# Kernel optimization log

Measured on AMD Instinct MI355X. Metric: run time of the kernel, lower is better.

## Reference

```python
import jax, jax.numpy as jnp
import numpy as np


def setup_inputs() -> dict:
    key = jax.random.key(0)
    ks = jax.random.split(key, 7)
    N, T, E = 4, 2048, 1024
    s = 1.0 / np.sqrt(E)
    return {
        "X": jax.random.normal(ks[0], (N, T, E), dtype=jnp.float32),
        "Wq": jax.random.normal(ks[1], (E, E), dtype=jnp.float32) * s,
        "bq": jax.random.normal(ks[2], (E,), dtype=jnp.float32) * 0.01,
        "Wk": jax.random.normal(ks[3], (E, E), dtype=jnp.float32) * s,
        "bk": jax.random.normal(ks[4], (E,), dtype=jnp.float32) * 0.01,
        "Wv": jax.random.normal(ks[5], (E, E), dtype=jnp.float32) * s,
        "bv": jax.random.normal(ks[6], (E,), dtype=jnp.float32) * 0.01,
    }


def reference(X, Wq, bq, Wk, bk, Wv, bv):
    # QKV projections: [N,T,E] @ [E,E] + [E]
    q = jnp.einsum("nte,ef->ntf", X, Wq) + bq
    k = jnp.einsum("nte,ef->ntf", X, Wk) + bk
    v = jnp.einsum("nte,ef->ntf", X, Wv) + bv
    # Unscaled full attention (module does NOT divide by sqrt(E))
    sim = jnp.einsum("nqe,nke->nqk", q, k)         # [N,T,T]
    weight = jax.nn.softmax(sim, axis=2)
    return jnp.einsum("nqk,nke->nqe", weight, v)    # [N,T,E]
```

## Files before the change

kernel.cpp:

```cpp
#include <hip/hip_runtime.h>

typedef unsigned short u16;
typedef unsigned int u32;
typedef float floatx4 __attribute__((ext_vector_type(4)));
typedef __bf16 bf16x8 __attribute__((ext_vector_type(8)));

__device__ __forceinline__ u16 bf16_rne(float x) {
  u32 u = __builtin_bit_cast(u32, x);
  return (u16)((u + 0x7FFFu + ((u >> 16) & 1u)) >> 16);
}
__device__ __forceinline__ float bf16f(u16 h) {
  u32 u = ((u32)h) << 16;
  return __builtin_bit_cast(float, u);
}
__device__ __forceinline__ void g2l16(const u16* g, u16* l) {
  __builtin_amdgcn_global_load_lds((const __attribute__((address_space(1))) u32*)g,
                                   (__attribute__((address_space(3))) u32*)l, 16, 0, 0);
}
__device__ __forceinline__ floatx4 mfma16(bf16x8 a, bf16x8 b, floatx4 c) {
  return __builtin_amdgcn_mfma_f32_16x16x32_bf16(a, b, c, 0, 0, 0);
}
#define SB() __builtin_amdgcn_sched_barrier(0)

__global__ void split_x_kernel(const float* __restrict__ X, u16* __restrict__ Xh,
                               u16* __restrict__ Xl, int n4) {
  int i = blockIdx.x * blockDim.x + threadIdx.x;
  int stride = gridDim.x * blockDim.x;
  for (; i < n4; i += stride) {
    float4 x = reinterpret_cast<const float4*>(X)[i];
    float v[4] = {x.x, x.y, x.z, x.w};
    u16 hh[4], ll[4];
#pragma unroll
    for (int j = 0; j < 4; ++j) {
      hh[j] = bf16_rne(v[j]);
      ll[j] = bf16_rne(v[j] - bf16f(hh[j]));
    }
    reinterpret_cast<ushort4*>(Xh)[i] = make_ushort4(hh[0], hh[1], hh[2], hh[3]);
    reinterpret_cast<ushort4*>(Xl)[i] = make_ushort4(ll[0], ll[1], ll[2], ll[3]);
  }
}

__global__ void wsplit_t_kernel(const float* __restrict__ W, u16* __restrict__ Th,
                                u16* __restrict__ Tl) {
  __shared__ float tile[32][33];
  int tx = threadIdx.x, ty = threadIdx.y;
  int f0 = blockIdx.x * 32, e0 = blockIdx.y * 32;
  tile[ty][tx] = W[(e0 + ty) * 1024 + f0 + tx];
  __syncthreads();
  float v = tile[tx][ty];
  u16 h = bf16_rne(v);
  Th[(f0 + ty) * 1024 + e0 + tx] = h;
  Tl[(f0 + ty) * 1024 + e0 + tx] = bf16_rne(v - bf16f(h));
}

template <int EPI>
__global__ __launch_bounds__(512, 2) void gemm8_split(
    const u16* __restrict__ Ah, const u16* __restrict__ Al,
    const u16* __restrict__ Bh, const u16* __restrict__ Bl,
    float* __restrict__ C, u16* __restrict__ Oh, u16* __restrict__ Ol,
    const float* __restrict__ b1, const float* __restrict__ b2, int NH,
    int N, int K, int lda, int ldb, long sA, long sB, long sC) {
  __shared__ u16 lds[2][4][256 * 32];
  const int tid = threadIdx.x;
  const int z = blockIdx.z;
  const int brow = blockIdx.y * 256;
  const int bcol = blockIdx.x * 256;
  const int w = tid >> 6, l = tid & 63;
  const int wm = w >> 2, wn = w & 3;
  const int fr = l & 15, kq = l >> 4;

  const u16* gA0 = Ah + (long)z * sA + (long)brow * lda;
  const u16* gA1 = Al + (long)z * sA + (long)brow * lda;
  const u16* gB0 = Bh + (long)z * sB + (long)bcol * ldb;
  const u16* gB1 = Bl + (long)z * sB + (long)bcol * ldb;

  const int r0 = tid >> 2, s0 = tid & 3;
  const int r1 = (tid + 512) >> 2, s1 = (tid + 512) & 3;
  const long aOff0 = (long)r0 * lda + ((s0 ^ ((r0 >> 1) & 3)) << 3);
  const long aOff1 = (long)r1 * lda + ((s1 ^ ((r1 >> 1) & 3)) << 3);
  const long bOff0 = (long)r0 * ldb + ((s0 ^ ((r0 >> 1) & 3)) << 3);
  const long bOff1 = (long)r1 * ldb + ((s1 ^ ((r1 >> 1) & 3)) << 3);
  const int d0 = tid * 8, d1 = (tid + 512) * 8;

  auto STAGE = [&](int b, int k0) {
    g2l16(gA0 + aOff0 + k0, &lds[b][0][d0]);
    g2l16(gA0 + aOff1 + k0, &lds[b][0][d1]);
    g2l16(gA1 + aOff0 + k0, &lds[b][1][d0]);
    g2l16(gA1 + aOff1 + k0, &lds[b][1][d1]);
    g2l16(gB0 + bOff0 + k0, &lds[b][2][d0]);
    g2l16(gB0 + bOff1 + k0, &lds[b][2][d1]);
    g2l16(gB1 + bOff0 + k0, &lds[b][3][d0]);
    g2l16(gB1 + bOff1 + k0, &lds[b][3][d1]);
  };

  int aoffs[8], boffs[4];
#pragma unroll
  for (int m = 0; m < 8; ++m) {
    int r = wm * 128 + m * 16 + fr;
    aoffs[m] = r * 32 + (((kq ^ (r >> 1)) & 3) << 3);
  }
#pragma unroll
  for (int n = 0; n < 4; ++n) {
    int r = wn * 64 + n * 16 + fr;
    boffs[n] = r * 32 + (((kq ^ (r >> 1)) & 3) << 3);
  }

  floatx4 acc[8][4];
#pragma unroll
  for (int m = 0; m < 8; ++m)
#pragma unroll
    for (int n = 0; n < 4; ++n)
#pragma unroll
      for (int j = 0; j < 4; ++j) acc[m][n][j] = 0.f;

  const int NT = K >> 5;
  STAGE(0, 0);
  STAGE(1, 32);
  SB();
  asm volatile("s_waitcnt vmcnt(8)" ::: "memory");
  SB(); __builtin_amdgcn_s_barrier(); SB();

  bf16x8 fa_h[4], fa_l[4], fb_h[4], fb_l[4];

  for (int t = 0; t < NT; ++t) {
    const int p = t & 1;
    const u16* LAh = &lds[p][0][0];
    const u16* LAl = &lds[p][1][0];
    const u16* LBh = &lds[p][2][0];
    const u16* LBl = &lds[p][3][0];

#pragma unroll
    for (int m = 0; m < 4; ++m) {
      fa_h[m] = *(const bf16x8*)(LAh + aoffs[m]);
      fa_l[m] = *(const bf16x8*)(LAl + aoffs[m]);
    }
#pragma unroll
    for (int n = 0; n < 2; ++n) {
      fb_h[n] = *(const bf16x8*)(LBh + boffs[n]);
      fb_l[n] = *(const bf16x8*)(LBl + boffs[n]);
    }
    SB(); __builtin_amdgcn_s_barrier();
    asm volatile("s_waitcnt lgkmcnt(0)" ::: "memory");
    SB();
    __builtin_amdgcn_s_setprio(1);
#pragma unroll
    for (int m = 0; m < 4; ++m)
#pragma unroll
      for (int n = 0; n < 2; ++n) {
        acc[m][n] = mfma16(fa_h[m], fb_h[n], acc[m][n]);
        acc[m][n] = mfma16(fa_h[m], fb_l[n], acc[m][n]);
        acc[m][n] = mfma16(fa_l[m], fb_h[n], acc[m][n]);
      }
    __builtin_amdgcn_s_setprio(0);
    SB(); __builtin_amdgcn_s_barrier(); SB();

#pragma unroll
    for (int n = 2; n < 4; ++n) {
      fb_h[n] = *(const bf16x8*)(LBh + boffs[n]);
      fb_l[n] = *(const bf16x8*)(LBl + boffs[n]);
    }
    SB(); __builtin_amdgcn_s_barrier();
    asm volatile("s_waitcnt lgkmcnt(0)" ::: "memory");
    SB();
    __builtin_amdgcn_s_setprio(1);
#pragma unroll
    for (int m = 0; m < 4; ++m)
#pragma unroll
      for (int n = 2; n < 4; ++n) {
        acc[m][n] = mfma16(fa_h[m], fb_h[n], acc[m][n]);
        acc[m][n] = mfma16(fa_h[m], fb_l[n], acc[m][n]);
        acc[m][n] = mfma16(fa_l[m], fb_h[n], acc[m][n]);
      }
    __builtin_amdgcn_s_setprio(0);
    SB(); __builtin_amdgcn_s_barrier(); SB();

#pragma unroll
    for (int m = 0; m < 4; ++m) {
      fa_h[m] = *(const bf16x8*)(LAh + aoffs[m + 4]);
      fa_l[m] = *(const bf16x8*)(LAl + aoffs[m + 4]);
    }
    SB(); __builtin_amdgcn_s_barrier();
    asm volatile("s_waitcnt lgkmcnt(0)" ::: "memory");
    SB();
    __builtin_amdgcn_s_setprio(1);
#pragma unroll
    for (int m = 0; m < 4; ++m)
#pragma unroll
      for (int n = 0; n < 2; ++n) {
        acc[m + 4][n] = mfma16(fa_h[m], fb_h[n], acc[m + 4][n]);
        acc[m + 4][n] = mfma16(fa_h[m], fb_l[n], acc[m + 4][n]);
        acc[m + 4][n] = mfma16(fa_l[m], fb_h[n], acc[m + 4][n]);
      }
    __builtin_amdgcn_s_setprio(0);
    SB(); __builtin_amdgcn_s_barrier(); SB();

    if (t + 2 < NT) STAGE(p, (t + 2) << 5);
    SB();
    __builtin_amdgcn_s_setprio(1);
#pragma unroll
    for (int m = 0; m < 4; ++m)
#pragma unroll
      for (int n = 2; n < 4; ++n) {
        acc[m + 4][n] = mfma16(fa_h[m], fb_h[n], acc[m + 4][n]);
        acc[m + 4][n] = mfma16(fa_h[m], fb_l[n], acc[m + 4][n]);
        acc[m + 4][n] = mfma16(fa_l[m], fb_h[n], acc[m + 4][n]);
      }
    __builtin_amdgcn_s_setprio(0);
    SB();
    if (t + 2 < NT) {
      asm volatile("s_waitcnt vmcnt(8)" ::: "memory");
    } else {
      asm volatile("s_waitcnt vmcnt(0)" ::: "memory");
    }
    SB(); __builtin_amdgcn_s_barrier(); SB();
  }

#pragma unroll
  for (int m = 0; m < 8; ++m)
#pragma unroll
    for (int n = 0; n < 4; ++n)
#pragma unroll
      for (int j = 0; j < 4; ++j) {
        int gr = brow + wm * 128 + m * 16 + kq * 4 + j;
        int gc = bcol + wn * 64 + n * 16 + fr;
        float v = acc[m][n][j];
        if (EPI == 0) {
          C[(long)z * sC + (long)gr * N + gc] = v;
        } else {
          v += (gc < NH) ? b1[gc] : b2[gc - NH];
          u16 h = bf16_rne(v);
          long idx = (long)gr * N + gc;
          Oh[idx] = h;
          Ol[idx] = bf16_rne(v - bf16f(h));
        }
      }
}

template <int EPI>
__global__ __launch_bounds__(512, 2) void gemm8_plain(
    const u16* __restrict__ A, const u16* __restrict__ B,
    float* __restrict__ C, u16* __restrict__ Oh, const float* __restrict__ bias,
    int N, int K, int lda, int ldb, long sA, long sB, long sC) {
  __shared__ u16 lds[2][24576];
  const int BOFF = 16384;
  const int tid = threadIdx.x;
  const int z = blockIdx.z;
  const int brow = blockIdx.y * 256;
  const int bcol = blockIdx.x * 128;
  const int w = tid >> 6, l = tid & 63;
  const int wm = w >> 2, wn = w & 3;
  const int fr = l & 15, kq = l >> 4;

  const u16* gA = A + (long)z * sA + (long)brow * lda;
  const u16* gB = B + (long)z * sB + (long)bcol * ldb;

  long aO[4], bO[2];
  int aD[4], bD[2];
#pragma unroll
  for (int i = 0; i < 4; ++i) {
    int c = tid + i * 512, r = c >> 3, s = c & 7;
    aO[i] = (long)r * lda + ((s ^ (r & 7)) << 3);
    aD[i] = c * 8;
  }
#pragma unroll
  for (int i = 0; i < 2; ++i) {
    int c = tid + i * 512, r = c >> 3, s = c & 7;
    bO[i] = (long)r * ldb + ((s ^ (r & 7)) << 3);
    bD[i] = BOFF + c * 8;
  }

  auto STAGE = [&](int b, int k0) {
#pragma unroll
    for (int i = 0; i < 4; ++i) g2l16(gA + aO[i] + k0, &lds[b][aD[i]]);
#pragma unroll
    for (int i = 0; i < 2; ++i) g2l16(gB + bO[i] + k0, &lds[b][bD[i]]);
  };

  int aoffs[8][2], boffs[2][2];
#pragma unroll
  for (int m = 0; m < 8; ++m) {
    int r = wm * 128 + m * 16 + fr;
#pragma unroll
    for (int k = 0; k < 2; ++k) aoffs[m][k] = r * 64 + ((((k * 4 + kq) ^ r) & 7) << 3);
  }
#pragma unroll
  for (int n = 0; n < 2; ++n) {
    int r = wn * 32 + n * 16 + fr;
#pragma unroll
    for (int k = 0; k < 2; ++k) boffs[n][k] = BOFF + r * 64 + ((((k * 4 + kq) ^ r) & 7) << 3);
  }

  floatx4 acc[8][2];
#pragma unroll
  for (int m = 0; m < 8; ++m)
#pragma unroll
    for (int n = 0; n < 2; ++n)
#pragma unroll
      for (int j = 0; j < 4; ++j) acc[m][n][j] = 0.f;

  const int NT = K >> 6;
  STAGE(0, 0);
  STAGE(1, 64);
  SB();
  asm volatile("s_waitcnt vmcnt(6)" ::: "memory");
  SB(); __builtin_amdgcn_s_barrier(); SB();

  bf16x8 fak[4][2], fb[2][2];

  for (int t = 0; t < NT; ++t) {
    const int p = t & 1;
    const u16* L = &lds[p][0];

#pragma unroll
    for (int m = 0; m < 4; ++m)
#pragma unroll
      for (int k = 0; k < 2; ++k) fak[m][k] = *(const bf16x8*)(L + aoffs[m][k]);
#pragma unroll
    for (int n = 0; n < 2; ++n)
#pragma unroll
      for (int k = 0; k < 2; ++k) fb[n][k] = *(const bf16x8*)(L + boffs[n][k]);
    SB(); __builtin_amdgcn_s_barrier();
    asm volatile("s_waitcnt lgkmcnt(0)" ::: "memory");
    SB();
    __builtin_amdgcn_s_setprio(1);
#pragma unroll
    for (int m = 0; m < 4; ++m)
#pragma unroll
      for (int n = 0; n < 2; ++n) {
        acc[m][n] = mfma16(fak[m][0], fb[n][0], acc[m][n]);
        acc[m][n] = mfma16(fak[m][1], fb[n][1], acc[m][n]);
      }
    __builtin_amdgcn_s_setprio(0);
    SB(); __builtin_amdgcn_s_barrier(); SB();

#pragma unroll
    for (int m = 0; m < 4; ++m)
#pragma unroll
      for (int k = 0; k < 2; ++k) fak[m][k] = *(const bf16x8*)(L + aoffs[m + 4][k]);
    SB(); __builtin_amdgcn_s_barrier();
    asm volatile("s_waitcnt lgkmcnt(0)" ::: "memory");
    SB();
    __builtin_amdgcn_s_setprio(1);
#pragma unroll
    for (int m = 0; m < 4; ++m)
#pragma unroll
      for (int n = 0; n < 2; ++n)
        acc[m + 4][n] = mfma16(fak[m][0], fb[n][0], acc[m + 4][n]);
    __builtin_amdgcn_s_setprio(0);
    SB(); __builtin_amdgcn_s_barrier(); SB();

    if (t + 2 < NT) STAGE(p, (t + 2) << 6);
    SB();
    __builtin_amdgcn_s_setprio(1);
#pragma unroll
    for (int m = 0; m < 4; ++m)
#pragma unroll
      for (int n = 0; n < 2; ++n)
        acc[m + 4][n] = mfma16(fak[m][1], fb[n][1], acc[m + 4][n]);
    __builtin_amdgcn_s_setprio(0);
    SB();
    if (t + 2 < NT) {
      asm volatile("s_waitcnt vmcnt(6)" ::: "memory");
    } else {
      asm volatile("s_waitcnt vmcnt(0)" ::: "memory");
    }
    SB(); __builtin_amdgcn_s_barrier(); SB();
  }

#pragma unroll
  for (int m = 0; m < 8; ++m)
#pragma unroll
    for (int n = 0; n < 2; ++n)
#pragma unroll
      for (int j = 0; j < 4; ++j) {
        int gr = brow + wm * 128 + m * 16 + kq * 4 + j;
        int gc = bcol + wn * 32 + n * 16 + fr;
        float v = acc[m][n][j];
        if (EPI == 0) {
          C[(long)z * sC + (long)gr * N + gc] = v;
        } else {
          v += bias[gc];
          long oi = ((long)((gr >> 11) * 1024 + gc)) * 2048 + (gr & 2047);
          Oh[oi] = bf16_rne(v);
        }
      }
}

__global__ __launch_bounds__(256) void softmax_kernel(const float* __restrict__ S,
                                                      u16* __restrict__ Wgt) {
  const long row = blockIdx.x;
  const float4* src = reinterpret_cast<const float4*>(S + row * 2048);
  const int t = threadIdx.x;
  float4 x0 = src[t];
  float4 x1 = src[t + 256];
  float m = fmaxf(fmaxf(fmaxf(x0.x, x0.y), fmaxf(x0.z, x0.w)),
                  fmaxf(fmaxf(x1.x, x1.y), fmaxf(x1.z, x1.w)));
#pragma unroll
  for (int s = 32; s > 0; s >>= 1) m = fmaxf(m, __shfl_xor(m, s));
  __shared__ float redm[4];
  __shared__ float reds[4];
  if ((t & 63) == 0) redm[t >> 6] = m;
  __syncthreads();
  m = fmaxf(fmaxf(redm[0], redm[1]), fmaxf(redm[2], redm[3]));
  float e[8];
  e[0] = __expf(x0.x - m); e[1] = __expf(x0.y - m);
  e[2] = __expf(x0.z - m); e[3] = __expf(x0.w - m);
  e[4] = __expf(x1.x - m); e[5] = __expf(x1.y - m);
  e[6] = __expf(x1.z - m); e[7] = __expf(x1.w - m);
  float s = ((e[0] + e[1]) + (e[2] + e[3])) + ((e[4] + e[5]) + (e[6] + e[7]));
#pragma unroll
  for (int k = 32; k > 0; k >>= 1) s += __shfl_xor(s, k);
  if ((t & 63) == 0) reds[t >> 6] = s;
  __syncthreads();
  s = (reds[0] + reds[1]) + (reds[2] + reds[3]);
  float inv = 1.f / s;
  u32* dst = reinterpret_cast<u32*>(Wgt + row * 2048);
  dst[2 * t] = (u32)bf16_rne(e[0] * inv) | ((u32)bf16_rne(e[1] * inv) << 16);
  dst[2 * t + 1] = (u32)bf16_rne(e[2] * inv) | ((u32)bf16_rne(e[3] * inv) << 16);
  dst[2 * (t + 256)] = (u32)bf16_rne(e[4] * inv) | ((u32)bf16_rne(e[5] * inv) << 16);
  dst[2 * (t + 256) + 1] = (u32)bf16_rne(e[6] * inv) | ((u32)bf16_rne(e[7] * inv) << 16);
}

extern "C" void kernel_launch(void* const* d_in, const int* in_sizes, int n_in,
                              void* d_out, int out_size, void* d_ws, size_t ws_size,
                              hipStream_t stream) {
  const float* X = (const float*)d_in[0];
  const float* Wq = (const float*)d_in[1];
  const float* bq = (const float*)d_in[2];
  const float* Wk = (const float*)d_in[3];
  const float* bk = (const float*)d_in[4];
  const float* Wv = (const float*)d_in[5];
  const float* bv = (const float*)d_in[6];
  float* out = (float*)d_out;

  char* ws = (char*)d_ws;
  const size_t MB = 1ull << 20;
  u16* Xh = (u16*)(ws + 0 * MB);
  u16* Xl = (u16*)(ws + 16 * MB);
  u16* Wqkh = (u16*)(ws + 32 * MB);
  u16* Wqkl = (u16*)(ws + 36 * MB);
  u16* Wvh = (u16*)(ws + 40 * MB);
  u16* Wvl = (u16*)(ws + 42 * MB);
  float* sim = (float*)(ws);
  u16* qkh = (u16*)(ws + 64 * MB);
  u16* qkl = (u16*)(ws + 96 * MB);
  u16* vt = (u16*)(ws + 128 * MB);
  u16* wb = (u16*)(ws + 64 * MB);

  split_x_kernel<<<4096, 256, 0, stream>>>(X, Xh, Xl, (8192 * 1024) / 4);
  wsplit_t_kernel<<<dim3(32, 32), dim3(32, 32), 0, stream>>>(Wq, Wqkh, Wqkl);
  wsplit_t_kernel<<<dim3(32, 32), dim3(32, 32), 0, stream>>>(Wk, Wqkh + 1024 * 1024,
                                                             Wqkl + 1024 * 1024);
  wsplit_t_kernel<<<dim3(32, 32), dim3(32, 32), 0, stream>>>(Wv, Wvh, Wvl);
  gemm8_split<1><<<dim3(8, 32, 1), 512, 0, stream>>>(
      Xh, Xl, Wqkh, Wqkl, nullptr, qkh, qkl, bq, bk, 1024,
      2048, 1024, 1024, 1024, 0, 0, 0);
  gemm8_plain<2><<<dim3(8, 32, 1), 512, 0, stream>>>(
      Xh, Wvh, nullptr, vt, bv, 1024, 1024, 1024, 1024, 0, 0, 0);
  gemm8_split<0><<<dim3(8, 8, 4), 512, 0, stream>>>(
      qkh, qkl, qkh + 1024, qkl + 1024, sim, nullptr, nullptr, nullptr, nullptr, 0,
      2048, 1024, 2048, 2048, 2048L * 2048, 2048L * 2048, 2048L * 2048);
  softmax_kernel<<<8192, 256, 0, stream>>>(sim, wb);
  gemm8_plain<0><<<dim3(8, 8, 4), 512, 0, stream>>>(
      wb, vt, out, nullptr, nullptr, 1024, 2048, 2048, 2048,
      2048L * 2048, 1024L * 2048, 2048L * 1024);
}
```

Before: 378.2 us.

## Reshape plain GEMM tiles to 128x256, add XCD block swizzle, reorder MFMAs

```diff
diff --git a/kernel.cpp b/kernel.cpp
--- a/kernel.cpp
+++ b/kernel.cpp
@@ -21,6 +21,21 @@
   return __builtin_amdgcn_mfma_f32_16x16x32_bf16(a, b, c, 0, 0, 0);
 }
 #define SB() __builtin_amdgcn_sched_barrier(0)
+
+__device__ __forceinline__ void xcd_swizzle(int& bx, int& by, int& bz) {
+  const int gx = gridDim.x, gy = gridDim.y;
+  int nb = gx * gy * gridDim.z;
+  int flat = blockIdx.x + gx * (blockIdx.y + gy * blockIdx.z);
+  int swz = flat;
+  if ((nb & 7) == 0) {
+    int cpx = nb >> 3;
+    swz = (flat & 7) * cpx + (flat >> 3);
+  }
+  bz = swz / (gx * gy);
+  int rem = swz - bz * gx * gy;
+  by = rem / gx;
+  bx = rem - by * gx;
+}
 
 __global__ void split_x_kernel(const float* __restrict__ X, u16* __restrict__ Xh,
                                u16* __restrict__ Xl, int n4) {
@@ -62,9 +77,11 @@
     int N, int K, int lda, int ldb, long sA, long sB, long sC) {
   __shared__ u16 lds[2][4][256 * 32];
   const int tid = threadIdx.x;
-  const int z = blockIdx.z;
-  const int brow = blockIdx.y * 256;
-  const int bcol = blockIdx.x * 256;
+  int bx, by, bz;
+  xcd_swizzle(bx, by, bz);
+  const int z = bz;
+  const int brow = by * 256;
+  const int bcol = bx * 256;
   const int w = tid >> 6, l = tid & 63;
   const int wm = w >> 2, wn = w & 3;
   const int fr = l & 15, kq = l >> 4;
@@ -146,11 +163,15 @@
 #pragma unroll
     for (int m = 0; m < 4; ++m)
 #pragma unroll
-      for (int n = 0; n < 2; ++n) {
-        acc[m][n] = mfma16(fa_h[m], fb_h[n], acc[m][n]);
-        acc[m][n] = mfma16(fa_h[m], fb_l[n], acc[m][n]);
-        acc[m][n] = mfma16(fa_l[m], fb_h[n], acc[m][n]);
-      }
+      for (int n = 0; n < 2; ++n) acc[m][n] = mfma16(fa_h[m], fb_h[n], acc[m][n]);
+#pragma unroll
+    for (int m = 0; m < 4; ++m)
+#pragma unroll
+      for (int n = 0; n < 2; ++n) acc[m][n] = mfma16(fa_h[m], fb_l[n], acc[m][n]);
+#pragma unroll
+    for (int m = 0; m < 4; ++m)
+#pragma unroll
+      for (int n = 0; n < 2; ++n) acc[m][n] = mfma16(fa_l[m], fb_h[n], acc[m][n]);
     __builtin_amdgcn_s_setprio(0);
     SB(); __builtin_amdgcn_s_barrier(); SB();
 
@@ -166,11 +187,15 @@
 #pragma unroll
     for (int m = 0; m < 4; ++m)
 #pragma unroll
-      for (int n = 2; n < 4; ++n) {
-        acc[m][n] = mfma16(fa_h[m], fb_h[n], acc[m][n]);
-        acc[m][n] = mfma16(fa_h[m], fb_l[n], acc[m][n]);
-        acc[m][n] = mfma16(fa_l[m], fb_h[n], acc[m][n]);
-      }
+      for (int n = 2; n < 4; ++n) acc[m][n] = mfma16(fa_h[m], fb_h[n], acc[m][n]);
+#pragma unroll
+    for (int m = 0; m < 4; ++m)
+#pragma unroll
+      for (int n = 2; n < 4; ++n) acc[m][n] = mfma16(fa_h[m], fb_l[n], acc[m][n]);
+#pragma unroll
+    for (int m = 0; m < 4; ++m)
+#pragma unroll
+      for (int n = 2; n < 4; ++n) acc[m][n] = mfma16(fa_l[m], fb_h[n], acc[m][n]);
     __builtin_amdgcn_s_setprio(0);
     SB(); __builtin_amdgcn_s_barrier(); SB();
 
@@ -186,11 +211,15 @@
 #pragma unroll
     for (int m = 0; m < 4; ++m)
 #pragma unroll
-      for (int n = 0; n < 2; ++n) {
-        acc[m + 4][n] = mfma16(fa_h[m], fb_h[n], acc[m + 4][n]);
-        acc[m + 4][n] = mfma16(fa_h[m], fb_l[n], acc[m + 4][n]);
-        acc[m + 4][n] = mfma16(fa_l[m], fb_h[n], acc[m + 4][n]);
-      }
+      for (int n = 0; n < 2; ++n) acc[m + 4][n] = mfma16(fa_h[m], fb_h[n], acc[m + 4][n]);
+#pragma unroll
+    for (int m = 0; m < 4; ++m)
+#pragma unroll
+      for (int n = 0; n < 2; ++n) acc[m + 4][n] = mfma16(fa_h[m], fb_l[n], acc[m + 4][n]);
+#pragma unroll
+    for (int m = 0; m < 4; ++m)
+#pragma unroll
+      for (int n = 0; n < 2; ++n) acc[m + 4][n] = mfma16(fa_l[m], fb_h[n], acc[m + 4][n]);
     __builtin_amdgcn_s_setprio(0);
     SB(); __builtin_amdgcn_s_barrier(); SB();
 
@@ -200,11 +229,15 @@
 #pragma unroll
     for (int m = 0; m < 4; ++m)
 #pragma unroll
-      for (int n = 2; n < 4; ++n) {
-        acc[m + 4][n] = mfma16(fa_h[m], fb_h[n], acc[m + 4][n]);
-        acc[m + 4][n] = mfma16(fa_h[m], fb_l[n], acc[m + 4][n]);
-        acc[m + 4][n] = mfma16(fa_l[m], fb_h[n], acc[m + 4][n]);
-      }
+      for (int n = 2; n < 4; ++n) acc[m + 4][n] = mfma16(fa_h[m], fb_h[n], acc[m + 4][n]);
+#pragma unroll
+    for (int m = 0; m < 4; ++m)
+#pragma unroll
+      for (int n = 2; n < 4; ++n) acc[m + 4][n] = mfma16(fa_h[m], fb_l[n], acc[m + 4][n]);
+#pragma unroll
+    for (int m = 0; m < 4; ++m)
+#pragma unroll
+      for (int n = 2; n < 4; ++n) acc[m + 4][n] = mfma16(fa_l[m], fb_h[n], acc[m + 4][n]);
     __builtin_amdgcn_s_setprio(0);
     SB();
     if (t + 2 < NT) {
@@ -242,28 +275,30 @@
     float* __restrict__ C, u16* __restrict__ Oh, const float* __restrict__ bias,
     int N, int K, int lda, int ldb, long sA, long sB, long sC) {
   __shared__ u16 lds[2][24576];
-  const int BOFF = 16384;
+  const int BOFF = 8192;
   const int tid = threadIdx.x;
-  const int z = blockIdx.z;
-  const int brow = blockIdx.y * 256;
-  const int bcol = blockIdx.x * 128;
+  int bx, by, bz;
+  xcd_swizzle(bx, by, bz);
+  const int z = bz;
+  const int brow = by * 128;
+  const int bcol = bx * 256;
   const int w = tid >> 6, l = tid & 63;
-  const int wm = w >> 2, wn = w & 3;
+  const int wm = (w >> 2) * 64, wn = (w & 3) * 64;
   const int fr = l & 15, kq = l >> 4;
 
   const u16* gA = A + (long)z * sA + (long)brow * lda;
   const u16* gB = B + (long)z * sB + (long)bcol * ldb;
 
-  long aO[4], bO[2];
-  int aD[4], bD[2];
-#pragma unroll
-  for (int i = 0; i < 4; ++i) {
+  long aO[2], bO[4];
+  int aD[2], bD[4];
+#pragma unroll
+  for (int i = 0; i < 2; ++i) {
     int c = tid + i * 512, r = c >> 3, s = c & 7;
     aO[i] = (long)r * lda + ((s ^ (r & 7)) << 3);
     aD[i] = c * 8;
   }
 #pragma unroll
-  for (int i = 0; i < 2; ++i) {
+  for (int i = 0; i < 4; ++i) {
     int c = tid + i * 512, r = c >> 3, s = c & 7;
     bO[i] = (long)r * ldb + ((s ^ (r & 7)) << 3);
     bD[i] = BOFF + c * 8;
@@ -271,30 +306,30 @@
 
   auto STAGE = [&](int b, int k0) {
 #pragma unroll
-    for (int i = 0; i < 4; ++i) g2l16(gA + aO[i] + k0, &lds[b][aD[i]]);
-#pragma unroll
-    for (int i = 0; i < 2; ++i) g2l16(gB + bO[i] + k0, &lds[b][bD[i]]);
+    for (int i = 0; i < 2; ++i) g2l16(gA + aO[i] + k0, &lds[b][aD[i]]);
+#pragma unroll
+    for (int i = 0; i < 4; ++i) g2l16(gB + bO[i] + k0, &lds[b][bD[i]]);
   };
 
-  int aoffs[8][2], boffs[2][2];
-#pragma unroll
-  for (int m = 0; m < 8; ++m) {
-    int r = wm * 128 + m * 16 + fr;
+  int aoffs[4][2], boffs[4][2];
+#pragma unroll
+  for (int m = 0; m < 4; ++m) {
+    int r = wm + m * 16 + fr;
 #pragma unroll
     for (int k = 0; k < 2; ++k) aoffs[m][k] = r * 64 + ((((k * 4 + kq) ^ r) & 7) << 3);
   }
 #pragma unroll
-  for (int n = 0; n < 2; ++n) {
-    int r = wn * 32 + n * 16 + fr;
+  for (int n = 0; n < 4; ++n) {
+    int r = wn + n * 16 + fr;
 #pragma unroll
     for (int k = 0; k < 2; ++k) boffs[n][k] = BOFF + r * 64 + ((((k * 4 + kq) ^ r) & 7) << 3);
   }
 
-  floatx4 acc[8][2];
-#pragma unroll
-  for (int m = 0; m < 8; ++m)
-#pragma unroll
-    for (int n = 0; n < 2; ++n)
+  floatx4 acc[4][4];
+#pragma unroll
+  for (int m = 0; m < 4; ++m)
+#pragma unroll
+    for (int n = 0; n < 4; ++n)
 #pragma unroll
       for (int j = 0; j < 4; ++j) acc[m][n][j] = 0.f;
 
@@ -305,16 +340,16 @@
   asm volatile("s_waitcnt vmcnt(6)" ::: "memory");
   SB(); __builtin_amdgcn_s_barrier(); SB();
 
-  bf16x8 fak[4][2], fb[2][2];
+  bf16x8 fa[2][2], fb[4][2];
 
   for (int t = 0; t < NT; ++t) {
     const int p = t & 1;
     const u16* L = &lds[p][0];
 
 #pragma unroll
-    for (int m = 0; m < 4; ++m)
-#pragma unroll
-      for (int k = 0; k < 2; ++k) fak[m][k] = *(const bf16x8*)(L + aoffs[m][k]);
+    for (int m = 0; m < 2; ++m)
+#pragma unroll
+      for (int k = 0; k < 2; ++k) fa[m][k] = *(const bf16x8*)(L + aoffs[m][k]);
 #pragma unroll
     for (int n = 0; n < 2; ++n)
 #pragma unroll
@@ -324,28 +359,51 @@
     SB();
     __builtin_amdgcn_s_setprio(1);
 #pragma unroll
-    for (int m = 0; m < 4; ++m)
-#pragma unroll
-      for (int n = 0; n < 2; ++n) {
-        acc[m][n] = mfma16(fak[m][0], fb[n][0], acc[m][n]);
-        acc[m][n] = mfma16(fak[m][1], fb[n][1], acc[m][n]);
-      }
-    __builtin_amdgcn_s_setprio(0);
-    SB(); __builtin_amdgcn_s_barrier(); SB();
-
-#pragma unroll
-    for (int m = 0; m < 4; ++m)
-#pragma unroll
-      for (int k = 0; k < 2; ++k) fak[m][k] = *(const bf16x8*)(L + aoffs[m + 4][k]);
+    for (int m = 0; m < 2; ++m)
+#pragma unroll
+      for (int n = 0; n < 2; ++n) acc[m][n] = mfma16(fa[m][0], fb[n][0], acc[m][n]);
+#pragma unroll
+    for (int m = 0; m < 2; ++m)
+#pragma unroll
+      for (int n = 0; n < 2; ++n) acc[m][n] = mfma16(fa[m][1], fb[n][1], acc[m][n]);
+    __builtin_amdgcn_s_setprio(0);
+    SB(); __builtin_amdgcn_s_barrier(); SB();
+
+#pragma unroll
+    for (int n = 2; n < 4; ++n)
+#pragma unroll
+      for (int k = 0; k < 2; ++k) fb[n][k] = *(const bf16x8*)(L + boffs[n][k]);
     SB(); __builtin_amdgcn_s_barrier();
     asm volatile("s_waitcnt lgkmcnt(0)" ::: "memory");
     SB();
     __builtin_amdgcn_s_setprio(1);
 #pragma unroll
-    for (int m = 0; m < 4; ++m)
-#pragma unroll
-      for (int n = 0; n < 2; ++n)
-        acc[m + 4][n] = mfma16(fak[m][0], fb[n][0], acc[m + 4][n]);
+    for (int m = 0; m < 2; ++m)
+#pragma unroll
+      for (int n = 2; n < 4; ++n) acc[m][n] = mfma16(fa[m][0], fb[n][0], acc[m][n]);
+#pragma unroll
+    for (int m = 0; m < 2; ++m)
+#pragma unroll
+      for (int n = 2; n < 4; ++n) acc[m][n] = mfma16(fa[m][1], fb[n][1], acc[m][n]);
+    __builtin_amdgcn_s_setprio(0);
+    SB(); __builtin_amdgcn_s_barrier(); SB();
+
+#pragma unroll
+    for (int m = 0; m < 2; ++m)
+#pragma unroll
+      for (int k = 0; k < 2; ++k) fa[m][k] = *(const bf16x8*)(L + aoffs[m + 2][k]);
+    SB(); __builtin_amdgcn_s_barrier();
+    asm volatile("s_waitcnt lgkmcnt(0)" ::: "memory");
+    SB();
+    __builtin_amdgcn_s_setprio(1);
+#pragma unroll
+    for (int m = 0; m < 2; ++m)
+#pragma unroll
+      for (int n = 0; n < 2; ++n) acc[m + 2][n] = mfma16(fa[m][0], fb[n][0], acc[m + 2][n]);
+#pragma unroll
+    for (int m = 0; m < 2; ++m)
+#pragma unroll
+      for (int n = 0; n < 2; ++n) acc[m + 2][n] = mfma16(fa[m][1], fb[n][1], acc[m + 2][n]);
     __builtin_amdgcn_s_setprio(0);
     SB(); __builtin_amdgcn_s_barrier(); SB();
 
@@ -353,10 +411,13 @@
     SB();
     __builtin_amdgcn_s_setprio(1);
 #pragma unroll
-    for (int m = 0; m < 4; ++m)
-#pragma unroll
-      for (int n = 0; n < 2; ++n)
-        acc[m + 4][n] = mfma16(fak[m][1], fb[n][1], acc[m + 4][n]);
+    for (int m = 0; m < 2; ++m)
+#pragma unroll
+      for (int n = 2; n < 4; ++n) acc[m + 2][n] = mfma16(fa[m][0], fb[n][0], acc[m + 2][n]);
+#pragma unroll
+    for (int m = 0; m < 2; ++m)
+#pragma unroll
+      for (int n = 2; n < 4; ++n) acc[m + 2][n] = mfma16(fa[m][1], fb[n][1], acc[m + 2][n]);
     __builtin_amdgcn_s_setprio(0);
     SB();
     if (t + 2 < NT) {
@@ -368,13 +429,13 @@
   }
 
 #pragma unroll
-  for (int m = 0; m < 8; ++m)
-#pragma unroll
-    for (int n = 0; n < 2; ++n)
+  for (int m = 0; m < 4; ++m)
+#pragma unroll
+    for (int n = 0; n < 4; ++n)
 #pragma unroll
       for (int j = 0; j < 4; ++j) {
-        int gr = brow + wm * 128 + m * 16 + kq * 4 + j;
-        int gc = bcol + wn * 32 + n * 16 + fr;
+        int gr = brow + wm + m * 16 + kq * 4 + j;
+        int gc = bcol + wn + n * 16 + fr;
         float v = acc[m][n][j];
         if (EPI == 0) {
           C[(long)z * sC + (long)gr * N + gc] = v;
@@ -455,13 +516,13 @@
   gemm8_split<1><<<dim3(8, 32, 1), 512, 0, stream>>>(
       Xh, Xl, Wqkh, Wqkl, nullptr, qkh, qkl, bq, bk, 1024,
       2048, 1024, 1024, 1024, 0, 0, 0);
-  gemm8_plain<2><<<dim3(8, 32, 1), 512, 0, stream>>>(
+  gemm8_plain<2><<<dim3(4, 64, 1), 512, 0, stream>>>(
       Xh, Wvh, nullptr, vt, bv, 1024, 1024, 1024, 1024, 0, 0, 0);
   gemm8_split<0><<<dim3(8, 8, 4), 512, 0, stream>>>(
       qkh, qkl, qkh + 1024, qkl + 1024, sim, nullptr, nullptr, nullptr, nullptr, 0,
       2048, 1024, 2048, 2048, 2048L * 2048, 2048L * 2048, 2048L * 2048);
   softmax_kernel<<<8192, 256, 0, stream>>>(sim, wb);
-  gemm8_plain<0><<<dim3(8, 8, 4), 512, 0, stream>>>(
+  gemm8_plain<0><<<dim3(4, 16, 4), 512, 0, stream>>>(
       wb, vt, out, nullptr, nullptr, 1024, 2048, 2048, 2048,
       2048L * 2048, 1024L * 2048, 2048L * 1024);
 }
```

Result: faster. 357.2 us (-5.5%).
